# Optimization experiments

Hardware: AMD Instinct MI355X
Metric: run time of the kernel (lower is better)

## Reference

```python
import jax, jax.numpy as jnp
import numpy as np

N_NODES = 100000


def _mean_agg(x, src, dst, n_nodes):
    # gather neighbor (src) features, segment-sum into destination nodes, divide by in-degree
    summed = jax.ops.segment_sum(x[src], dst, num_segments=n_nodes)  # [N, d]
    deg = jax.ops.segment_sum(jnp.ones_like(dst, dtype=x.dtype), dst, num_segments=n_nodes)
    return summed / jnp.clip(deg, 1.0)[:, None]  # DGL clamps zero in-degree to 1


def _sage_conv(x, src, dst, W_self, W_neigh, b, n_nodes):
    h_neigh = _mean_agg(x, src, dst, n_nodes)
    # DGL SAGEConv(mean): fc_self(h_self) + fc_neigh(h_neigh); single bias
    return x @ W_self + h_neigh @ W_neigh + b


def setup_inputs() -> dict:
    key = jax.random.key(0)
    ks = jax.random.split(key, 8)
    in_f, hid_f, out_f = 64, 64, 16
    n_edges = 1200000
    return {
        "x": jax.random.normal(ks[0], (N_NODES, in_f), dtype=jnp.float32),
        "src": jax.random.randint(ks[1], (n_edges,), 0, N_NODES),
        "dst": jax.random.randint(ks[2], (n_edges,), 0, N_NODES),
        "W1_self": jax.random.normal(ks[3], (in_f, hid_f), dtype=jnp.float32) / np.sqrt(in_f),
        "W1_neigh": jax.random.normal(ks[4], (in_f, hid_f), dtype=jnp.float32) / np.sqrt(in_f),
        "b1": jnp.zeros((hid_f,), dtype=jnp.float32),
        "W2_self": jax.random.normal(ks[5], (hid_f, out_f), dtype=jnp.float32) / np.sqrt(hid_f),
        "W2_neigh": jax.random.normal(ks[6], (hid_f, out_f), dtype=jnp.float32) / np.sqrt(hid_f),
        "b2": jnp.zeros((out_f,), dtype=jnp.float32),
    }


def reference(x, src, dst, W1_self, W1_neigh, b1, W2_self, W2_neigh, b2):
    h = _sage_conv(x, src, dst, W1_self, W1_neigh, b1, N_NODES)
    h = jax.nn.relu(h)
    h = _sage_conv(h, src, dst, W2_self, W2_neigh, b2, N_NODES)
    return h
```

## Files before the change

### kernel.cpp

```cpp
#include <hip/hip_runtime.h>

#define N_NODES 100000
#define N_EDGES 1200000
#define BK 64
#define NB 1563
#define CHUNK_E 4096
#define NBLK_E 293
#define TOT_H (NB * NBLK_E)
#define NSB2 ((TOT_H + 1023) / 1024)
#define CAP 1536
#define ND1 3125

#define OFF_ROWPTR 0
#define OFF_HISTG  401408
#define OFF_BLK2   2234368
#define OFF_PAIRS  2236416
#define OFF_SORTED 7036928
#define OFF_Y1     11837440
#define OFF_H1     24637440

__device__ __forceinline__ unsigned short f2bf(float f) {
    unsigned u = __float_as_uint(f);
    unsigned r = (u + 0x7fffu + ((u >> 16) & 1u)) >> 16;
    return (unsigned short)r;
}

__global__ __launch_bounds__(256) void hist_dense1_kernel(
    const int* __restrict__ dst, int* __restrict__ hist_g,
    const float* __restrict__ x,
    const float* __restrict__ Wn, const float* __restrict__ Ws,
    const float* __restrict__ b,
    unsigned short* __restrict__ y1, float* __restrict__ z1)
{
    __shared__ float sx[32 * 64];
    const int t = threadIdx.x;

    if (blockIdx.x < NBLK_E) {
        int* h = (int*)sx;
        const int e0 = blockIdx.x * CHUNK_E;
        const int e1 = min(e0 + CHUNK_E, N_EDGES);
        for (int i = t; i < NB; i += 256) h[i] = 0;
        __syncthreads();
        for (int e = e0 + t; e < e1; e += 256)
            atomicAdd(&h[dst[e] >> 6], 1);
        __syncthreads();
        for (int i = t; i < NB; i += 256)
            hist_g[i * NBLK_E + blockIdx.x] = h[i];
        return;
    }

    const int bid = blockIdx.x - NBLK_E;
    const int w = t >> 6;
    const int lane = t & 63;
    const int half = w >> 1;
    const int nsub = (w & 1) * 16;
    const int chunk = bid * 32;

    {
        const float4* gx = (const float4*)(x + (size_t)chunk * 64);
        float4* sx4 = (float4*)sx;
        sx4[t] = gx[t];
        sx4[t + 256] = gx[t + 256];
    }

    const float* W = half ? Ws : Wn;
    float wr[64];
#pragma unroll
    for (int k = 0; k < 64; ++k) wr[k] = W[k * 64 + lane];
    const float bj = half ? b[lane] : 0.f;

    __syncthreads();

#pragma unroll 1
    for (int m = 0; m < 16; ++m) {
        const int node = nsub + m;
        const float4* xr = (const float4*)(sx + node * 64);
        float a0 = 0.f, a1 = 0.f, a2 = 0.f, a3 = 0.f;
#pragma unroll
        for (int k4 = 0; k4 < 16; ++k4) {
            float4 v = xr[k4];
            a0 += v.x * wr[4 * k4 + 0];
            a1 += v.y * wr[4 * k4 + 1];
            a2 += v.z * wr[4 * k4 + 2];
            a3 += v.w * wr[4 * k4 + 3];
        }
        const float o = (a0 + a1) + (a2 + a3) + bj;
        const size_t gn = (size_t)(chunk + node);
        if (half) z1[gn * 64 + lane] = o;
        else      y1[gn * 64 + lane] = f2bf(o);
    }
}

__global__ __launch_bounds__(1024) void scan2_blocks_kernel(
    int* __restrict__ hist_g, int* __restrict__ blk2)
{
    __shared__ int s[1024];
    int i = blockIdx.x * 1024 + threadIdx.x;
    int v = (i < TOT_H) ? hist_g[i] : 0;
    s[threadIdx.x] = v;
    __syncthreads();
    for (int off = 1; off < 1024; off <<= 1) {
        int tv = (threadIdx.x >= off) ? s[threadIdx.x - off] : 0;
        __syncthreads();
        s[threadIdx.x] += tv;
        __syncthreads();
    }
    if (i < TOT_H) hist_g[i] = s[threadIdx.x] - v;
    if (threadIdx.x == 1023) blk2[blockIdx.x] = s[1023];
}

__device__ __forceinline__ void local_tops_scan(const int* blk2, int* tops, int t)
{
    int v = (t < NSB2) ? blk2[t] : 0;
    tops[t] = v;
    __syncthreads();
    for (int off = 1; off < 512; off <<= 1) {
        int tv = (t >= off) ? tops[t - off] : 0;
        __syncthreads();
        tops[t] += tv;
        __syncthreads();
    }
    int ex = tops[t] - v;
    __syncthreads();
    tops[t] = ex;
    __syncthreads();
}

__global__ __launch_bounds__(512) void pair_scatter_kernel(
    const int* __restrict__ src, const int* __restrict__ dst,
    const int* __restrict__ hs_scan, const int* __restrict__ blk2,
    unsigned* __restrict__ pairs)
{
    __shared__ int base_s[NB];
    __shared__ int cur_s[NB];
    __shared__ int tops[512];
    const int b = blockIdx.x;
    const int t = threadIdx.x;
    const int e0 = b * CHUNK_E;
    const int e1 = min(e0 + CHUNK_E, N_EDGES);

    local_tops_scan(blk2, tops, t);

    for (int i = t; i < NB; i += 512) {
        int idx = i * NBLK_E + b;
        base_s[i] = hs_scan[idx] + tops[idx >> 10];
        cur_s[i] = 0;
    }
    __syncthreads();
    for (int e = e0 + t; e < e1; e += 512) {
        int d = dst[e];
        int bk = d >> 6;
        int pos = base_s[bk] + atomicAdd(&cur_s[bk], 1);
        pairs[pos] = ((unsigned)src[e] << 6) | (unsigned)(d & 63);
    }
}

__global__ __launch_bounds__(512) void fused_gather1_kernel(
    const unsigned short* __restrict__ y1,
    const unsigned* __restrict__ pairs,
    const int* __restrict__ hs_scan, const int* __restrict__ blk2,
    int* __restrict__ row_ptr, int* __restrict__ sorted_src,
    float* __restrict__ h1)
{
    __shared__ int slist[CAP];
    __shared__ int hist[BK];
    __shared__ int sc[BK];
    __shared__ int cur[BK];
    __shared__ int tops[512];
    const int b = blockIdx.x;
    const int t = threadIdx.x;

    local_tops_scan(blk2, tops, t);

    const int i0 = b * NBLK_E;
    const int start = hs_scan[i0] + tops[i0 >> 10];
    const int end = (b == NB - 1) ? N_EDGES
                    : hs_scan[i0 + NBLK_E] + tops[(i0 + NBLK_E) >> 10];
    const int cnt = end - start;
    const int node0 = b * BK;

    if (t < BK) hist[t] = 0;
    __syncthreads();
    for (int e = start + t; e < end; e += 512)
        atomicAdd(&hist[pairs[e] & 63u], 1);
    __syncthreads();

    int v = (t < BK) ? hist[t] : 0;
    if (t < BK) sc[t] = v;
    __syncthreads();
    for (int off = 1; off < BK; off <<= 1) {
        int tv = (t >= off && t < BK) ? sc[t - off] : 0;
        __syncthreads();
        if (t < BK) sc[t] += tv;
        __syncthreads();
    }
    const int excl = (t < BK) ? sc[t] - v : 0;
    if (t < BK && node0 + t < N_NODES) row_ptr[node0 + t] = start + excl;
    if (b == NB - 1 && t == 0) row_ptr[N_NODES] = N_EDGES;
    if (t < BK) cur[t] = excl;
    __syncthreads();

    const int wv = t >> 6;
    const int lane = t & 63;
    const int sub = lane >> 5;
    const int sl = lane & 31;
    const int eg = sl >> 3;
    const int fl = sl & 7;

    if (cnt <= CAP) {
        for (int e = start + t; e < end; e += 512) {
            unsigned u = pairs[e];
            int p = atomicAdd(&cur[u & 63u], 1);
            slist[p] = (int)(u >> 6);
        }
        __syncthreads();
        for (int i = t; i < cnt; i += 512)
            sorted_src[start + i] = slist[i];
        for (int q = 0; q < 4; ++q) {
            const int node = wv * 8 + q * 2 + sub;
            const int gn = node0 + node;
            if (gn >= N_NODES) break;
            const int o = sc[node] - hist[node];
            const int dg = hist[node];
            float4* hp = (float4*)(h1 + (size_t)gn * 64);
            float4 z;
            if (eg < 2) z = hp[fl * 2 + eg];
            float a0 = 0.f, a1 = 0.f, a2 = 0.f, a3 = 0.f;
            float a4 = 0.f, a5 = 0.f, a6 = 0.f, a7 = 0.f;
            for (int base = 0; base < dg; base += 8) {
                const int i0e = base + eg;
                const int i1e = base + 4 + eg;
                const bool v0 = i0e < dg, v1 = i1e < dg;
                uint4 r0, r1;
                if (v0) {
                    const int s = slist[o + i0e];
                    r0 = ((const uint4*)(y1 + (size_t)s * 64))[fl];
                }
                if (v1) {
                    const int s = slist[o + i1e];
                    r1 = ((const uint4*)(y1 + (size_t)s * 64))[fl];
                }
                if (v0) {
                    a0 += __uint_as_float(r0.x << 16);
                    a1 += __uint_as_float(r0.x & 0xffff0000u);
                    a2 += __uint_as_float(r0.y << 16);
                    a3 += __uint_as_float(r0.y & 0xffff0000u);
                    a4 += __uint_as_float(r0.z << 16);
                    a5 += __uint_as_float(r0.z & 0xffff0000u);
                    a6 += __uint_as_float(r0.w << 16);
                    a7 += __uint_as_float(r0.w & 0xffff0000u);
                }
                if (v1) {
                    a0 += __uint_as_float(r1.x << 16);
                    a1 += __uint_as_float(r1.x & 0xffff0000u);
                    a2 += __uint_as_float(r1.y << 16);
                    a3 += __uint_as_float(r1.y & 0xffff0000u);
                    a4 += __uint_as_float(r1.z << 16);
                    a5 += __uint_as_float(r1.z & 0xffff0000u);
                    a6 += __uint_as_float(r1.w << 16);
                    a7 += __uint_as_float(r1.w & 0xffff0000u);
                }
            }
#pragma unroll
            for (int d = 8; d <= 16; d <<= 1) {
                a0 += __shfl_xor(a0, d); a1 += __shfl_xor(a1, d);
                a2 += __shfl_xor(a2, d); a3 += __shfl_xor(a3, d);
                a4 += __shfl_xor(a4, d); a5 += __shfl_xor(a5, d);
                a6 += __shfl_xor(a6, d); a7 += __shfl_xor(a7, d);
            }
            const float invd = 1.0f / (float)max(dg, 1);
            if (eg == 0) {
                hp[fl * 2] = make_float4(fmaxf(z.x + a0 * invd, 0.f),
                                         fmaxf(z.y + a1 * invd, 0.f),
                                         fmaxf(z.z + a2 * invd, 0.f),
                                         fmaxf(z.w + a3 * invd, 0.f));
            } else if (eg == 1) {
                hp[fl * 2 + 1] = make_float4(fmaxf(z.x + a4 * invd, 0.f),
                                             fmaxf(z.y + a5 * invd, 0.f),
                                             fmaxf(z.z + a6 * invd, 0.f),
                                             fmaxf(z.w + a7 * invd, 0.f));
            }
        }
    } else {
        if (t < BK) cur[t] = start + excl;
        __syncthreads();
        for (int e = start + t; e < end; e += 512) {
            unsigned u = pairs[e];
            int p = atomicAdd(&cur[u & 63u], 1);
            sorted_src[p] = (int)(u >> 6);
        }
        __syncthreads();
        for (int q = 0; q < 4; ++q) {
            const int node = wv * 8 + q * 2 + sub;
            const int gn = node0 + node;
            if (gn >= N_NODES) break;
            const int o = start + sc[node] - hist[node];
            const int dg = hist[node];
            float4* hp = (float4*)(h1 + (size_t)gn * 64);
            float4 z;
            if (eg < 2) z = hp[fl * 2 + eg];
            float a0 = 0.f, a1 = 0.f, a2 = 0.f, a3 = 0.f;
            float a4 = 0.f, a5 = 0.f, a6 = 0.f, a7 = 0.f;
            for (int base = 0; base < dg; base += 4) {
                const int idx = base + eg;
                if (idx < dg) {
                    const int s = sorted_src[o + idx];
                    uint4 raw = ((const uint4*)(y1 + (size_t)s * 64))[fl];
                    a0 += __uint_as_float(raw.x << 16);
                    a1 += __uint_as_float(raw.x & 0xffff0000u);
                    a2 += __uint_as_float(raw.y << 16);
                    a3 += __uint_as_float(raw.y & 0xffff0000u);
                    a4 += __uint_as_float(raw.z << 16);
                    a5 += __uint_as_float(raw.z & 0xffff0000u);
                    a6 += __uint_as_float(raw.w << 16);
                    a7 += __uint_as_float(raw.w & 0xffff0000u);
                }
            }
#pragma unroll
            for (int d = 8; d <= 16; d <<= 1) {
                a0 += __shfl_xor(a0, d); a1 += __shfl_xor(a1, d);
                a2 += __shfl_xor(a2, d); a3 += __shfl_xor(a3, d);
                a4 += __shfl_xor(a4, d); a5 += __shfl_xor(a5, d);
                a6 += __shfl_xor(a6, d); a7 += __shfl_xor(a7, d);
            }
            const float invd = 1.0f / (float)max(dg, 1);
            if (eg == 0) {
                hp[fl * 2] = make_float4(fmaxf(z.x + a0 * invd, 0.f),
                                         fmaxf(z.y + a1 * invd, 0.f),
                                         fmaxf(z.z + a2 * invd, 0.f),
                                         fmaxf(z.w + a3 * invd, 0.f));
            } else if (eg == 1) {
                hp[fl * 2 + 1] = make_float4(fmaxf(z.x + a4 * invd, 0.f),
                                             fmaxf(z.y + a5 * invd, 0.f),
                                             fmaxf(z.z + a6 * invd, 0.f),
                                             fmaxf(z.w + a7 * invd, 0.f));
            }
        }
    }
}

__global__ __launch_bounds__(256) void dense2_kernel(
    const float* __restrict__ h1,
    const float* __restrict__ Wn, const float* __restrict__ Ws,
    const float* __restrict__ b,
    float* __restrict__ y2, float* __restrict__ out)
{
    __shared__ float sx[32 * 68];
    const int t = threadIdx.x;
    const int w = t >> 6;
    const int lane = t & 63;
    const int half = w >> 1;
    const int nsub = (w & 1) * 16;
    const int j = lane & 15;
    const int g = lane >> 4;
    const int chunk = blockIdx.x * 32;

    {
        const float4* gx = (const float4*)(h1 + (size_t)chunk * 64);
        float4* sx4 = (float4*)sx;
        int r0 = t >> 4, c0 = t & 15;
        sx4[r0 * 17 + c0] = gx[t];
        sx4[(r0 + 16) * 17 + c0] = gx[t + 256];
    }

    const float* W = half ? Ws : Wn;
    float wr[64];
#pragma unroll
    for (int k = 0; k < 64; ++k) wr[k] = W[k * 16 + j];
    const float bj = half ? b[j] : 0.f;

    __syncthreads();

#pragma unroll 1
    for (int q = 0; q < 4; ++q) {
        const int node = nsub + q * 4 + g;
        const float4* xr = (const float4*)(sx + node * 68);
        float a0 = 0.f, a1 = 0.f, a2 = 0.f, a3 = 0.f;
#pragma unroll
        for (int k4 = 0; k4 < 16; ++k4) {
            float4 v = xr[k4];
            a0 += v.x * wr[4 * k4 + 0];
            a1 += v.y * wr[4 * k4 + 1];
            a2 += v.z * wr[4 * k4 + 2];
            a3 += v.w * wr[4 * k4 + 3];
        }
        const float o = (a0 + a1) + (a2 + a3) + bj;
        const size_t gn = (size_t)(chunk + node);
        if (half) out[gn * 16 + j] = o;
        else      y2[gn * 16 + j] = o;
    }
}

__global__ __launch_bounds__(256) void gather2_kernel(
    const float* __restrict__ y2,
    const int* __restrict__ row_ptr,
    const int* __restrict__ sorted_src,
    float* __restrict__ out)
{
    const int wv = threadIdx.x >> 6;
    const int lane = threadIdx.x & 63;
    const int sub = lane >> 4;
    const int sl = lane & 15;
    const int eg = sl >> 2;
    const int fl = sl & 3;

    const int n = blockIdx.x * 16 + wv * 4 + sub;
    const int start = row_ptr[n];
    const int deg = row_ptr[n + 1] - start;

    float4* op = (float4*)(out + (size_t)n * 16);
    float4 z;
    if (eg == 0) z = op[fl];

    float4 acc = make_float4(0.f, 0.f, 0.f, 0.f);
    for (int base = 0; base < deg; base += 16) {
        int eid = 0;
        if (base + sl < deg) eid = sorted_src[start + base + sl];
#pragma unroll
        for (int jj = 0; jj < 16; jj += 4) {
            const int idx = jj + eg;
            const int s = __shfl(eid, sub * 16 + idx);
            if (base + idx < deg) {
                float4 v = ((const float4*)(y2 + (size_t)s * 16))[fl];
                acc.x += v.x; acc.y += v.y; acc.z += v.z; acc.w += v.w;
            }
        }
    }
#pragma unroll
    for (int d = 4; d <= 8; d <<= 1) {
        acc.x += __shfl_xor(acc.x, d); acc.y += __shfl_xor(acc.y, d);
        acc.z += __shfl_xor(acc.z, d); acc.w += __shfl_xor(acc.w, d);
    }
    const float invd = 1.0f / (float)max(deg, 1);
    if (eg == 0) {
        op[fl] = make_float4(z.x + acc.x * invd, z.y + acc.y * invd,
                             z.z + acc.z * invd, z.w + acc.w * invd);
    }
}

extern "C" void kernel_launch(void* const* d_in, const int* in_sizes, int n_in,
                              void* d_out, int out_size, void* d_ws, size_t ws_size,
                              hipStream_t stream) {
    const float* x   = (const float*)d_in[0];
    const int*   src = (const int*)d_in[1];
    const int*   dst = (const int*)d_in[2];
    const float* W1s = (const float*)d_in[3];
    const float* W1n = (const float*)d_in[4];
    const float* b1  = (const float*)d_in[5];
    const float* W2s = (const float*)d_in[6];
    const float* W2n = (const float*)d_in[7];
    const float* b2  = (const float*)d_in[8];
    float* out = (float*)d_out;

    char* ws = (char*)d_ws;
    int* row_ptr    = (int*)(ws + OFF_ROWPTR);
    int* hist_g     = (int*)(ws + OFF_HISTG);
    int* blk2       = (int*)(ws + OFF_BLK2);
    unsigned* pairs = (unsigned*)(ws + OFF_PAIRS);
    int* sorted_src = (int*)(ws + OFF_SORTED);
    unsigned short* y1 = (unsigned short*)(ws + OFF_Y1);
    float* y2       = (float*)(ws + OFF_Y1);
    float* h1       = (float*)(ws + OFF_H1);

    hist_dense1_kernel<<<NBLK_E + ND1, 256, 0, stream>>>(
        dst, hist_g, x, W1n, W1s, b1, y1, h1);
    scan2_blocks_kernel<<<NSB2, 1024, 0, stream>>>(hist_g, blk2);
    pair_scatter_kernel<<<NBLK_E, 512, 0, stream>>>(src, dst, hist_g, blk2, pairs);
    fused_gather1_kernel<<<NB, 512, 0, stream>>>(y1, pairs, hist_g, blk2,
                                                 row_ptr, sorted_src, h1);
    dense2_kernel<<<ND1, 256, 0, stream>>>(h1, W2n, W2s, b2, y2, out);
    gather2_kernel<<<N_NODES / 16, 256, 0, stream>>>(y2, row_ptr, sorted_src, out);
}
```

Before: 219.0 us.

## Stage dense-layer weights in LDS and register-block over nodes instead of weight registers

Both dense kernels stop holding a 64-entry weight column in registers per thread. They stage the weight matrices in shared memory and swap the loop order, so each loaded weight quadruple is reused across several node accumulators. Layer-1 dense work is split into separate blocks for the self and neighbour weights, doubling that grid, and each block now loads x twice across the pair. The goal is lower register pressure and higher occupancy, at the cost of more LDS traffic, extra shared memory per block and duplicated x loads.

```diff
diff --git a/kernel.cpp b/kernel.cpp
--- a/kernel.cpp
+++ b/kernel.cpp
@@ -9,7 +9,8 @@
 #define TOT_H (NB * NBLK_E)
 #define NSB2 ((TOT_H + 1023) / 1024)
 #define CAP 1536
-#define ND1 3125
+#define NDB 6250
+#define ND2 3125
 
 #define OFF_ROWPTR 0
 #define OFF_HISTG  401408
@@ -33,6 +34,7 @@
     unsigned short* __restrict__ y1, float* __restrict__ z1)
 {
     __shared__ float sx[32 * 64];
+    __shared__ float sW[64 * 64];
     const int t = threadIdx.x;
 
     if (blockIdx.x < NBLK_E) {
@@ -49,43 +51,44 @@
         return;
     }
 
-    const int bid = blockIdx.x - NBLK_E;
+    const int db = blockIdx.x - NBLK_E;
+    const int half = db & 1;
+    const int chunk = (db >> 1) * 32;
     const int w = t >> 6;
     const int lane = t & 63;
-    const int half = w >> 1;
-    const int nsub = (w & 1) * 16;
-    const int chunk = bid * 32;
 
     {
         const float4* gx = (const float4*)(x + (size_t)chunk * 64);
         float4* sx4 = (float4*)sx;
         sx4[t] = gx[t];
         sx4[t + 256] = gx[t + 256];
-    }
-
-    const float* W = half ? Ws : Wn;
-    float wr[64];
-#pragma unroll
-    for (int k = 0; k < 64; ++k) wr[k] = W[k * 64 + lane];
+        const float4* gW = (const float4*)(half ? Ws : Wn);
+        float4* sW4 = (float4*)sW;
+#pragma unroll
+        for (int i = 0; i < 4; ++i) sW4[t + 256 * i] = gW[t + 256 * i];
+    }
     const float bj = half ? b[lane] : 0.f;
 
     __syncthreads();
 
+    const int n0 = w * 8;
+    float acc[8] = {0.f, 0.f, 0.f, 0.f, 0.f, 0.f, 0.f, 0.f};
 #pragma unroll 1
-    for (int m = 0; m < 16; ++m) {
-        const int node = nsub + m;
-        const float4* xr = (const float4*)(sx + node * 64);
-        float a0 = 0.f, a1 = 0.f, a2 = 0.f, a3 = 0.f;
-#pragma unroll
-        for (int k4 = 0; k4 < 16; ++k4) {
-            float4 v = xr[k4];
-            a0 += v.x * wr[4 * k4 + 0];
-            a1 += v.y * wr[4 * k4 + 1];
-            a2 += v.z * wr[4 * k4 + 2];
-            a3 += v.w * wr[4 * k4 + 3];
-        }
-        const float o = (a0 + a1) + (a2 + a3) + bj;
-        const size_t gn = (size_t)(chunk + node);
+    for (int k4 = 0; k4 < 16; ++k4) {
+        const float w0 = sW[(4 * k4 + 0) * 64 + lane];
+        const float w1 = sW[(4 * k4 + 1) * 64 + lane];
+        const float w2 = sW[(4 * k4 + 2) * 64 + lane];
+        const float w3 = sW[(4 * k4 + 3) * 64 + lane];
+#pragma unroll
+        for (int m = 0; m < 8; ++m) {
+            const float4 v = ((const float4*)(sx + (n0 + m) * 64))[k4];
+            acc[m] += v.x * w0 + v.y * w1 + v.z * w2 + v.w * w3;
+        }
+    }
+#pragma unroll
+    for (int m = 0; m < 8; ++m) {
+        const float o = acc[m] + bj;
+        const size_t gn = (size_t)(chunk + n0 + m);
         if (half) z1[gn * 64 + lane] = o;
         else      y1[gn * 64 + lane] = f2bf(o);
     }
@@ -346,6 +349,7 @@
     float* __restrict__ y2, float* __restrict__ out)
 {
     __shared__ float sx[32 * 68];
+    __shared__ float sW2[2 * 1024];
     const int t = threadIdx.x;
     const int w = t >> 6;
     const int lane = t & 63;
@@ -361,31 +365,31 @@
         int r0 = t >> 4, c0 = t & 15;
         sx4[r0 * 17 + c0] = gx[t];
         sx4[(r0 + 16) * 17 + c0] = gx[t + 256];
-    }
-
-    const float* W = half ? Ws : Wn;
-    float wr[64];
-#pragma unroll
-    for (int k = 0; k < 64; ++k) wr[k] = W[k * 16 + j];
+        ((float4*)sW2)[t] = ((const float4*)Wn)[t];
+        ((float4*)sW2)[256 + t] = ((const float4*)Ws)[t];
+    }
     const float bj = half ? b[j] : 0.f;
-
-    __syncthreads();
-
+    const float* sWh = sW2 + half * 1024;
+
+    __syncthreads();
+
+    float acc[4] = {0.f, 0.f, 0.f, 0.f};
 #pragma unroll 1
+    for (int k4 = 0; k4 < 16; ++k4) {
+        const float w0 = sWh[(4 * k4 + 0) * 16 + j];
+        const float w1 = sWh[(4 * k4 + 1) * 16 + j];
+        const float w2 = sWh[(4 * k4 + 2) * 16 + j];
+        const float w3 = sWh[(4 * k4 + 3) * 16 + j];
+#pragma unroll
+        for (int q = 0; q < 4; ++q) {
+            const float4 v = ((const float4*)(sx + (nsub + q * 4 + g) * 68))[k4];
+            acc[q] += v.x * w0 + v.y * w1 + v.z * w2 + v.w * w3;
+        }
+    }
+#pragma unroll
     for (int q = 0; q < 4; ++q) {
-        const int node = nsub + q * 4 + g;
-        const float4* xr = (const float4*)(sx + node * 68);
-        float a0 = 0.f, a1 = 0.f, a2 = 0.f, a3 = 0.f;
-#pragma unroll
-        for (int k4 = 0; k4 < 16; ++k4) {
-            float4 v = xr[k4];
-            a0 += v.x * wr[4 * k4 + 0];
-            a1 += v.y * wr[4 * k4 + 1];
-            a2 += v.z * wr[4 * k4 + 2];
-            a3 += v.w * wr[4 * k4 + 3];
-        }
-        const float o = (a0 + a1) + (a2 + a3) + bj;
-        const size_t gn = (size_t)(chunk + node);
+        const float o = acc[q] + bj;
+        const size_t gn = (size_t)(chunk + nsub + q * 4 + g);
         if (half) out[gn * 16 + j] = o;
         else      y2[gn * 16 + j] = o;
     }
@@ -462,12 +466,12 @@
     float* y2       = (float*)(ws + OFF_Y1);
     float* h1       = (float*)(ws + OFF_H1);
 
-    hist_dense1_kernel<<<NBLK_E + ND1, 256, 0, stream>>>(
+    hist_dense1_kernel<<<NBLK_E + NDB, 256, 0, stream>>>(
         dst, hist_g, x, W1n, W1s, b1, y1, h1);
     scan2_blocks_kernel<<<NSB2, 1024, 0, stream>>>(hist_g, blk2);
     pair_scatter_kernel<<<NBLK_E, 512, 0, stream>>>(src, dst, hist_g, blk2, pairs);
     fused_gather1_kernel<<<NB, 512, 0, stream>>>(y1, pairs, hist_g, blk2,
                                                  row_ptr, sorted_src, h1);
-    dense2_kernel<<<ND1, 256, 0, stream>>>(h1, W2n, W2s, b2, y2, out);
+    dense2_kernel<<<ND2, 256, 0, stream>>>(h1, W2n, W2s, b2, y2, out);
     gather2_kernel<<<N_NODES / 16, 256, 0, stream>>>(y2, row_ptr, sorted_src, out);
 }
```

After: 222.8 us. About the same (+1.7%).
